# Kernel tuning notes

Measured on AMD Instinct MI355X. Metric: run time of the kernel, lower is better.

The kernel has to match this reference:

```python
import jax, jax.numpy as jnp
import numpy as np

# dims
B, NN, D, HD, L, H, S, FIN = 2048, 64, 128, 128, 4, 8, 8, 16
N = B * NN              # total nodes = 131072
EPG = 8 * NN            # edges per graph (avg degree 8)
E = B * EPG             # total edges = 1048576
A = S * (S - 1)         # num_actions per head = 56


def setup_inputs() -> dict:
    key = jax.random.key(0)
    ks = jax.random.split(key, 16)
    def nrm(k, shape, scale=0.05):
        return jax.random.normal(k, shape, jnp.float32) * scale
    x = jax.random.normal(ks[0], (N, FIN), jnp.float32)
    # per-graph random edges (src/dst local in [0, NN), offset by graph id)
    off = jnp.repeat(jnp.arange(B, dtype=jnp.int32) * NN, EPG)
    src = jax.random.randint(ks[1], (E,), 0, NN, jnp.int32) + off
    dst = jax.random.randint(ks[2], (E,), 0, NN, jnp.int32) + off
    edge_index = jnp.stack([src, dst])
    batch = (jnp.arange(N, dtype=jnp.int32) // NN)
    subsets = jnp.arange(H * S, dtype=jnp.int32).reshape(H, S)
    return dict(
        x=x, edge_index=edge_index, batch=batch, subsets=subsets,
        W_in=nrm(ks[3], (FIN, D)), b_in=jnp.zeros(D, jnp.float32),
        W_self=nrm(ks[4], (L, D, D)), W_nbr=nrm(ks[5], (L, D, D)),
        b_enc=jnp.zeros((L, D), jnp.float32),
        ext_W=nrm(ks[6], (H, 2 * D, HD)), ext_b=jnp.zeros((H, HD), jnp.float32),
        ln_g=jnp.ones((H, HD), jnp.float32), ln_b=jnp.zeros((H, HD), jnp.float32),
        hub_W=nrm(ks[7], (HD, HD)), hub_b=jnp.zeros(HD, jnp.float32),
        pol_W1=nrm(ks[8], (H, 2 * HD, HD)), pol_b1=jnp.zeros((H, HD), jnp.float32),
        pol_W2=nrm(ks[9], (H, HD, A)), pol_b2=jnp.zeros((H, A), jnp.float32),
        val_W1=nrm(ks[10], (D, D)), val_b1=jnp.zeros(D, jnp.float32),
        val_W2=nrm(ks[11], (D, 1)), val_b2=jnp.zeros(1, jnp.float32),
    )


def _forward(floats, edge_index, batch, subsets):
    (x, W_in, b_in, W_self, W_nbr, b_enc, ext_W, ext_b, ln_g, ln_b,
     hub_W, hub_b, pol_W1, pol_b1, pol_W2, pol_b2,
     val_W1, val_b1, val_W2, val_b2) = floats
    src, dst = edge_index[0], edge_index[1]
    # --- GraphEncoder: input proj + L layers of mean-aggregate message passing ---
    deg = jnp.maximum(
        jax.ops.segment_sum(jnp.ones(src.shape[0], x.dtype), dst, num_segments=N), 1.0
    )[:, None]
    h = jax.nn.relu(x @ W_in + b_in)                      # [N, D]
    for l in range(L):
        agg = jax.ops.segment_sum(h[src], dst, num_segments=N) / deg
        h = jax.nn.relu(h @ W_self[l] + agg @ W_nbr[l] + b_enc[l])
    # --- batched per-graph / per-head subset pooling (replaces python loop) ---
    he = h.reshape(B, NN, D)                              # graphs are contiguous in `batch`
    sub = he[:, subsets]                                  # [B, H, S, D]
    pooled = jnp.concatenate([sub.mean(2), sub.max(2)], axis=-1)   # [B, H, 2D]
    z = jnp.einsum('bhf,hfd->bhd', pooled, ext_W) + ext_b
    mu = z.mean(-1, keepdims=True)
    var = z.var(-1, keepdims=True)
    head_emb = jax.nn.relu((z - mu) / jnp.sqrt(var + 1e-5) * ln_g + ln_b)  # [B, H, HD]
    # --- CommunicationHub: shared global context from mean over heads ---
    ctx = jax.nn.relu(head_emb.mean(1) @ hub_W + hub_b)   # [B, HD]
    # --- PolicyHeads: per-head MLP on concat(head_emb, context) ---
    pc = jnp.concatenate(
        [head_emb, jnp.broadcast_to(ctx[:, None, :], head_emb.shape)], axis=-1)
    hh = jax.nn.relu(jnp.einsum('bhf,hfd->bhd', pc, pol_W1) + pol_b1)
    logits = jnp.einsum('bhd,hda->bha', hh, pol_W2) + pol_b2       # [B, H, A]
    # --- ValueHead: per-graph mean pool -> MLP -> tanh ---
    gm = he.mean(1)                                        # segment mean (equal-size graphs)
    v = jnp.tanh(jax.nn.relu(gm @ val_W1 + val_b1) @ val_W2 + val_b2)  # [B, 1]
    return logits, v


def reference(x, edge_index, batch, subsets, W_in, b_in, W_self, W_nbr, b_enc,
              ext_W, ext_b, ln_g, ln_b, hub_W, hub_b, pol_W1, pol_b1, pol_W2,
              pol_b2, val_W1, val_b1, val_W2, val_b2):
    floats = (x, W_in, b_in, W_self, W_nbr, b_enc, ext_W, ext_b, ln_g, ln_b,
              hub_W, hub_b, pol_W1, pol_b1, pol_W2, pol_b2,
              val_W1, val_b1, val_W2, val_b2)
    return _forward(floats, edge_index, batch, subsets)
```

## Files before the change

### kernel.cpp

```cpp
#include <hip/hip_runtime.h>

#define E_TOT 1048576
#define LOGITS 917504

typedef short bf16x8 __attribute__((ext_vector_type(8)));
typedef float f32x4 __attribute__((ext_vector_type(4)));
typedef unsigned short u16;
typedef unsigned int u32;

#define DEV static __device__ __forceinline__

DEV u16 f2bf(float f){ u32 u = __float_as_uint(f); return (u16)((u + 0x7fffu + ((u>>16)&1u))>>16); }
DEV float bf2f(u16 h){ return __uint_as_float(((u32)h)<<16); }
DEV u32 pack2(float a, float b){ return (u32)f2bf(a) | ((u32)f2bf(b)<<16); }
DEV void unpack8(uint4 u, float* f){
  f[0]=__uint_as_float(u.x<<16); f[1]=__uint_as_float(u.x&0xffff0000u);
  f[2]=__uint_as_float(u.y<<16); f[3]=__uint_as_float(u.y&0xffff0000u);
  f[4]=__uint_as_float(u.z<<16); f[5]=__uint_as_float(u.z&0xffff0000u);
  f[6]=__uint_as_float(u.w<<16); f[7]=__uint_as_float(u.w&0xffff0000u);
}
DEV uint4 pack8(const float* f){
  uint4 u; u.x=pack2(f[0],f[1]); u.y=pack2(f[2],f[3]); u.z=pack2(f[4],f[5]); u.w=pack2(f[6],f[7]); return u;
}

#define GNN_E   0
#define EXT_E   131072
#define POL1_E  393216
#define POL2_E  655360
#define HUB_E   720896
#define VW1T_E  737280
#define POOL_E  753664
#define CTX_E   4947968

__global__ __launch_bounds__(256) void pack_w(
    const float* __restrict__ Wself, const float* __restrict__ Wnbr,
    const float* __restrict__ extW,  const float* __restrict__ polW1,
    const float* __restrict__ polW2, const float* __restrict__ hubW,
    const float* __restrict__ valW1, const float* __restrict__ W_in,
    u16* __restrict__ ws)
{
  int idx = blockIdx.x*256 + threadIdx.x;
  if (idx < 131072){
    int l = idx>>15, r = idx&32767;
    int m = (r>>14)&1, r2 = r&16383;
    int kb=(r2>>12)&3, ct=(r2>>9)&7, lane=(r2>>3)&63, j=r2&7;
    int k = kb*32 + ((lane>>4)<<3) + j, n = (ct<<4)+(lane&15);
    const float* W = m? Wnbr : Wself;
    ws[GNN_E+idx] = f2bf(W[(l<<14)+(k<<7)+n]);
  } else if (idx < 655360){
    int i = idx - 131072;
    int isPol = (i >= 262144); if (isPol) i -= 262144;
    int h = i>>15, r = i&32767;
    int kb=(r>>12)&7, ct=(r>>9)&7, lane=(r>>3)&63, j=r&7;
    int k = kb*32 + ((lane>>4)<<3) + j, n = (ct<<4)+(lane&15);
    const float* W = isPol? polW1 : extW;
    ws[(isPol?POL1_E:EXT_E)+i] = f2bf(W[(h<<15)+(k<<7)+n]);
  } else if (idx < 720896){
    int i = idx - 655360;
    int h = i>>13, r = i&8191;
    int kb=(r>>11)&3, ct=(r>>9)&3, lane=(r>>3)&63, j=r&7;
    int k = kb*32+((lane>>4)<<3)+j, n=(ct<<4)+(lane&15);
    float v = (n<56)? polW2[h*7168 + k*56 + n] : 0.0f;
    ws[POL2_E+i] = f2bf(v);
  } else if (idx < 737280){
    int i = idx-720896;
    int kb=(i>>12)&3, ct=(i>>9)&7, lane=(i>>3)&63, j=i&7;
    int k = kb*32+((lane>>4)<<3)+j, n=(ct<<4)+(lane&15);
    ws[HUB_E+i] = f2bf(hubW[(k<<7)+n]);
  } else if (idx < 753664){
    int i = idx-737280;
    int c = i>>7, k = i&127;
    ws[VW1T_E+i] = f2bf(valW1[(k<<7)+c]);
  } else if (idx < 757760){
    int i = idx-753664;
    int ct=(i>>9)&7, lane=(i>>3)&63, j=i&7;
    int k=((lane>>4)<<3)+j, n=(ct<<4)+(lane&15);
    float v = (k<16)? W_in[(k<<7)+n] : 0.0f;
    ws[CTX_E+i] = f2bf(v);
  }
}

DEV void epi_write(u16* h_bf, u16* ht, f32x4 (&acc)[4][2], float b0, float b1,
                   int wv, int r15, int kh)
{
  float bias[2] = {b0, b1};
  #pragma unroll
  for (int rt=0;rt<4;rt++){
    int sch = (rt<<1)+(kh>>1);
    int r0  = (rt<<4)+(kh<<2);
    #pragma unroll
    for (int cc=0;cc<2;cc++){
      int col=(wv<<5)+(cc<<4)+r15;
      float v0=fmaxf(acc[rt][cc][0]+bias[cc],0.0f);
      float v1=fmaxf(acc[rt][cc][1]+bias[cc],0.0f);
      float v2=fmaxf(acc[rt][cc][2]+bias[cc],0.0f);
      float v3=fmaxf(acc[rt][cc][3]+bias[cc],0.0f);
      int chc=(col>>3);
      h_bf[((r0+0)<<7)+(((chc^((r0+0)&7))<<3)|(col&7))]=f2bf(v0);
      h_bf[((r0+1)<<7)+(((chc^((r0+1)&7))<<3)|(col&7))]=f2bf(v1);
      h_bf[((r0+2)<<7)+(((chc^((r0+2)&7))<<3)|(col&7))]=f2bf(v2);
      h_bf[((r0+3)<<7)+(((chc^((r0+3)&7))<<3)|(col&7))]=f2bf(v3);
      uint2 w; w.x=pack2(v0,v1); w.y=pack2(v2,v3);
      *(uint2*)&ht[(col<<6)+(((sch^(col&7))<<3)|((kh&1)<<2))]=w;
    }
  }
}

__global__ __launch_bounds__(256,3) void gnn_kernel(
  const float* __restrict__ x, const int* __restrict__ ei,
  const int* __restrict__ subsets, const float* __restrict__ b_in,
  const float* __restrict__ b_enc, const float* __restrict__ val_b1,
  const float* __restrict__ val_W2, const float* __restrict__ val_b2,
  const u16* __restrict__ packGNN, const u16* __restrict__ packWIN,
  const u16* __restrict__ valW1T,
  u16* __restrict__ pooled, float* __restrict__ out)
{
  __shared__ __align__(16) u16 h_bf[8192];
  __shared__ __align__(16) u16 ht[8192];
  __shared__ __align__(16) u16 agg_bf[8192];
  __shared__ float deg_inv[64];
  __shared__ int subs_s[64];
  __shared__ float redbuf[4];

  int t=threadIdx.x, b=blockIdx.x;
  int lane=t&63, wv=t>>6, r15=lane&15, kh=lane>>4, ctb=wv<<1;
  u32* cnt=(u32*)ht;
  f32x4 zero4={0.0f,0.0f,0.0f,0.0f};

  int e0=(b<<9)+(t<<1);
  int2 sp=*(const int2*)&ei[e0];
  int2 dp=*(const int2*)&ei[E_TOT+e0];
  int s0=sp.x&63, s1=sp.y&63, d0=dp.x&63, d1=dp.y&63;
  if (t<64) subs_s[t]=subsets[t];
  for (int i=t;i<1024;i+=256) ((uint4*)cnt)[i]=make_uint4(0,0,0,0);
  __syncthreads();
  atomicAdd(&cnt[(d0<<6)+((((s0>>3)^(d0&7))<<3)|(s0&7))],1u);
  atomicAdd(&cnt[(d1<<6)+((((s1>>3)^(d1&7))<<3)|(s1&7))],1u);
  __syncthreads();
  if (t<64){
    u32 s=0;
    for (int k2=0;k2<16;k2++){ uint4 v=((uint4*)cnt)[(t<<4)+k2]; s+=v.x+v.y+v.z+v.w; }
    deg_inv[t]=1.0f/(float)(s>0u?s:1u);
  }
  __syncthreads();

  bf16x8 adjf[4][2];
  #pragma unroll
  for (int ct=0;ct<4;ct++){
    int dst=(ct<<4)+r15; float di=deg_inv[dst];
    #pragma unroll
    for (int kb=0;kb<2;kb++){
      int cb=(kb<<2)+kh;
      const u32* p=&cnt[(dst<<6)+((cb^(dst&7))<<3)];
      uint4 lo=*(const uint4*)p, hi=*(const uint4*)(p+4);
      bf16x8 v;
      v[0]=(short)f2bf((float)lo.x*di); v[1]=(short)f2bf((float)lo.y*di);
      v[2]=(short)f2bf((float)lo.z*di); v[3]=(short)f2bf((float)lo.w*di);
      v[4]=(short)f2bf((float)hi.x*di); v[5]=(short)f2bf((float)hi.y*di);
      v[6]=(short)f2bf((float)hi.z*di); v[7]=(short)f2bf((float)hi.w*di);
      adjf[ct][kb]=v;
    }
  }
  u16* xb=agg_bf;
  { const float* xg=x+(b<<10);
    for (int i=t;i<2048;i+=256){
      int row=i>>5, col=i&31;
      float v=(col<16)? xg[(row<<4)+col] : 0.0f;
      xb[(row<<5)+((((col>>3)^(row&3))<<3)|(col&7))]=f2bf(v);
    }
  }
  __syncthreads();

  {
    bf16x8 bw0=*(const bf16x8*)&packWIN[(ctb<<9)+(lane<<3)];
    bf16x8 bw1=*(const bf16x8*)&packWIN[((ctb+1)<<9)+(lane<<3)];
    f32x4 acc[4][2];
    #pragma unroll
    for (int rt=0;rt<4;rt++){ acc[rt][0]=zero4; acc[rt][1]=zero4; }
    #pragma unroll
    for (int rt=0;rt<4;rt++){
      int row=(rt<<4)+r15;
      bf16x8 af=*(const bf16x8*)&xb[(row<<5)+((kh^(row&3))<<3)];
      acc[rt][0]=__builtin_amdgcn_mfma_f32_16x16x32_bf16(af,bw0,acc[rt][0],0,0,0);
      acc[rt][1]=__builtin_amdgcn_mfma_f32_16x16x32_bf16(af,bw1,acc[rt][1],0,0,0);
    }
    float bi0=b_in[(wv<<5)+r15], bi1=b_in[(wv<<5)+16+r15];
    epi_write(h_bf,ht,acc,bi0,bi1,wv,r15,kh);
  }
  __syncthreads();

  #pragma unroll 1
  for (int l=0;l<4;l++){
    const u16* pl = packGNN + (l<<15);
    bf16x8 bs[4][2], bn[4][2];
    #pragma unroll
    for (int kb=0;kb<4;kb++){
      #pragma unroll
      for (int cc=0;cc<2;cc++){
        bs[kb][cc] = *(const bf16x8*)&pl[(kb<<12)+((ctb+cc)<<9)+(lane<<3)];
        bn[kb][cc] = *(const bf16x8*)&pl[16384+(kb<<12)+((ctb+cc)<<9)+(lane<<3)];
      }
    }
    f32x4 a2[2][4];
    #pragma unroll
    for (int rt=0;rt<2;rt++){ a2[rt][0]=zero4; a2[rt][1]=zero4; a2[rt][2]=zero4; a2[rt][3]=zero4; }
    #pragma unroll
    for (int kb=0;kb<2;kb++){
      #pragma unroll
      for (int rt=0;rt<2;rt++){
        int dim=((ctb+rt)<<4)+r15;
        bf16x8 af=*(const bf16x8*)&ht[(dim<<6)+((((kb<<2)+kh)^(dim&7))<<3)];
        #pragma unroll
        for (int ct=0;ct<4;ct++)
          a2[rt][ct]=__builtin_amdgcn_mfma_f32_16x16x32_bf16(af,adjf[ct][kb],a2[rt][ct],0,0,0);
      }
    }
    #pragma unroll
    for (int rt=0;rt<2;rt++){
      int dch=((ctb+rt)<<1)+(kh>>1);
      #pragma unroll
      for (int ct=0;ct<4;ct++){
        int node=(ct<<4)+r15;
        uint2 w; w.x=pack2(a2[rt][ct][0],a2[rt][ct][1]); w.y=pack2(a2[rt][ct][2],a2[rt][ct][3]);
        *(uint2*)&agg_bf[(node<<7)+(((dch^(node&7))<<3)|((kh&1)<<2))]=w;
      }
    }
    __syncthreads();
    f32x4 acc[4][2];
    #pragma unroll
    for (int rt=0;rt<4;rt++){ acc[rt][0]=zero4; acc[rt][1]=zero4; }
    #pragma unroll
    for (int kb=0;kb<4;kb++){
      int ch=(kb<<2)+kh;
      #pragma unroll
      for (int rt=0;rt<4;rt++){
        int row=(rt<<4)+r15;
        bf16x8 af=*(const bf16x8*)&h_bf[(row<<7)+((ch^(row&7))<<3)];
        acc[rt][0]=__builtin_amdgcn_mfma_f32_16x16x32_bf16(af,bs[kb][0],acc[rt][0],0,0,0);
        acc[rt][1]=__builtin_amdgcn_mfma_f32_16x16x32_bf16(af,bs[kb][1],acc[rt][1],0,0,0);
      }
      #pragma unroll
      for (int rt=0;rt<4;rt++){
        int row=(rt<<4)+r15;
        bf16x8 ag=*(const bf16x8*)&agg_bf[(row<<7)+((ch^(row&7))<<3)];
        acc[rt][0]=__builtin_amdgcn_mfma_f32_16x16x32_bf16(ag,bn[kb][0],acc[rt][0],0,0,0);
        acc[rt][1]=__builtin_amdgcn_mfma_f32_16x16x32_bf16(ag,bn[kb][1],acc[rt][1],0,0,0);
      }
    }
    float be0=b_enc[(l<<7)+(wv<<5)+r15], be1=b_enc[(l<<7)+(wv<<5)+16+r15];
    __syncthreads();
    epi_write(h_bf,ht,acc,be0,be1,wv,r15,kh);
    __syncthreads();
  }

  {
    int hd=t>>5, q=t&31, cb=q<<2;
    float ms[4]={0,0,0,0}, mx[4]={-3e38f,-3e38f,-3e38f,-3e38f};
    int ch=cb>>3;
    #pragma unroll
    for (int s=0;s<8;s++){
      int row=subs_s[(hd<<3)+s]; int sw=row&7;
      uint2 u=*(const uint2*)&h_bf[(row<<7)+(((ch^sw)<<3)|(cb&7))];
      float f0=__uint_as_float(u.x<<16), f1=__uint_as_float(u.x&0xffff0000u);
      float f2=__uint_as_float(u.y<<16), f3=__uint_as_float(u.y&0xffff0000u);
      ms[0]+=f0; ms[1]+=f1; ms[2]+=f2; ms[3]+=f3;
      mx[0]=fmaxf(mx[0],f0); mx[1]=fmaxf(mx[1],f1);
      mx[2]=fmaxf(mx[2],f2); mx[3]=fmaxf(mx[3],f3);
    }
    int base=(((b<<3)+hd)<<8);
    uint2 um,ux;
    um.x=pack2(ms[0]*0.125f,ms[1]*0.125f); um.y=pack2(ms[2]*0.125f,ms[3]*0.125f);
    ux.x=pack2(mx[0],mx[1]);               ux.y=pack2(mx[2],mx[3]);
    *(uint2*)&pooled[base+cb]    =um;
    *(uint2*)&pooled[base+128+cb]=ux;
  }
  __syncthreads();

  float* stagef=(float*)agg_bf;
  if (t<128){
    float s=0;
    for (int row=0;row<64;row++)
      s += bf2f(h_bf[(row<<7)+((((t>>3)^(row&7))<<3)|(t&7))]);
    stagef[t]=s*0.015625f;
  }
  __syncthreads();
  if (t<128){
    float acc=val_b1[t];
    const u16* wr=&valW1T[t<<7];
    #pragma unroll 8
    for (int k=0;k<128;k++) acc=fmaf(stagef[k],bf2f(wr[k]),acc);
    float contrib=fmaxf(acc,0.0f)*val_W2[t];
    #pragma unroll
    for (int d=1;d<64;d<<=1) contrib+=__shfl_xor(contrib,d);
    if (lane==0) redbuf[wv]=contrib;
  }
  __syncthreads();
  if (t==0) out[LOGITS+b]=tanhf(redbuf[0]+redbuf[1]+val_b2[0]);
}

__global__ __launch_bounds__(256) void head1_kernel(
  u16* __restrict__ pooled, const u16* __restrict__ packExt,
  const float* __restrict__ ext_b, const float* __restrict__ ln_g,
  const float* __restrict__ ln_b)
{
  __shared__ __align__(16) u16 A_lds[4096];
  __shared__ float zf[16*132];
  int t=threadIdx.x, gb=blockIdx.x, hd=blockIdx.y;
  int lane=t&63, wv=t>>6, r15=lane&15, kh=lane>>4, ctb=wv<<1;
  for (int i=t;i<512;i+=256){
    int row=i>>5, ch=i&31;
    uint4 u=*(const uint4*)&pooled[(((((gb<<4)+row)<<3)+hd)<<8)+(ch<<3)];
    *(uint4*)&A_lds[(row<<8)+((ch^(row&7))<<3)]=u;
  }
  __syncthreads();
  const u16* pw=packExt+(hd<<15);
  bf16x8 bw[8][2];
  #pragma unroll
  for (int kb=0;kb<8;kb++){
    bw[kb][0]=*(const bf16x8*)&pw[(kb<<12)+(ctb<<9)+(lane<<3)];
    bw[kb][1]=*(const bf16x8*)&pw[(kb<<12)+((ctb+1)<<9)+(lane<<3)];
  }
  f32x4 zero4={0.0f,0.0f,0.0f,0.0f};
  f32x4 acc[2]={zero4,zero4};
  #pragma unroll
  for (int kb=0;kb<8;kb++){
    int ch=(kb<<2)+kh;
    bf16x8 a=*(const bf16x8*)&A_lds[(r15<<8)+((ch^(r15&7))<<3)];
    acc[0]=__builtin_amdgcn_mfma_f32_16x16x32_bf16(a,bw[kb][0],acc[0],0,0,0);
    acc[1]=__builtin_amdgcn_mfma_f32_16x16x32_bf16(a,bw[kb][1],acc[1],0,0,0);
  }
  float eb[2]={ext_b[(hd<<7)+(wv<<5)+r15], ext_b[(hd<<7)+(wv<<5)+16+r15]};
  #pragma unroll
  for (int cc=0;cc<2;cc++){
    int col=(wv<<5)+(cc<<4)+r15;
    #pragma unroll
    for (int i=0;i<4;i++) zf[((kh<<2)+i)*132+col]=acc[cc][i]+eb[cc];
  }
  __syncthreads();
  int row=t>>4, q=t&15;
  const float* zr=&zf[row*132+(q<<3)];
  float s=0,ss=0;
  #pragma unroll
  for (int i=0;i<8;i++){ float v=zr[i]; s+=v; ss+=v*v; }
  s+=__shfl_xor(s,1); ss+=__shfl_xor(ss,1);
  s+=__shfl_xor(s,2); ss+=__shfl_xor(ss,2);
  s+=__shfl_xor(s,4); ss+=__shfl_xor(ss,4);
  s+=__shfl_xor(s,8); ss+=__shfl_xor(ss,8);
  float mu=s*0.0078125f, var=ss*0.0078125f-mu*mu, rstd=rsqrtf(var+1e-5f);
  const float* g=&ln_g[(hd<<7)+(q<<3)];
  const float* bb=&ln_b[(hd<<7)+(q<<3)];
  float e[8];
  #pragma unroll
  for (int i=0;i<8;i++) e[i]=fmaxf((zr[i]-mu)*rstd*g[i]+bb[i],0.0f);
  *(uint4*)&pooled[(((((gb<<4)+row)<<3)+hd)<<8)+(q<<3)]=pack8(e);
}

__global__ __launch_bounds__(256) void ctx_kernel(
  const u16* __restrict__ pooled, const u16* __restrict__ packHub,
  const float* __restrict__ hub_b, u16* __restrict__ ctx)
{
  __shared__ __align__(16) u16 m_lds[2048];
  int t=threadIdx.x, gb=blockIdx.x;
  int lane=t&63, wv=t>>6, r15=lane&15, kh=lane>>4, ctb=wv<<1;
  {
    int row=t>>4, ch=t&15;
    float a8[8]={0,0,0,0,0,0,0,0};
    #pragma unroll
    for (int h=0;h<8;h++){
      uint4 u=*(const uint4*)&pooled[(((((gb<<4)+row)<<3)+h)<<8)+(ch<<3)];
      float f[8]; unpack8(u,f);
      #pragma unroll
      for (int k=0;k<8;k++) a8[k]+=f[k];
    }
    #pragma unroll
    for (int k=0;k<8;k++) a8[k]*=0.125f;
    *(uint4*)&m_lds[(row<<7)+((ch^(row&7))<<3)]=pack8(a8);
  }
  __syncthreads();
  bf16x8 bh[4][2];
  #pragma unroll
  for (int kb=0;kb<4;kb++){
    bh[kb][0]=*(const bf16x8*)&packHub[(kb<<12)+(ctb<<9)+(lane<<3)];
    bh[kb][1]=*(const bf16x8*)&packHub[(kb<<12)+((ctb+1)<<9)+(lane<<3)];
  }
  f32x4 zero4={0.0f,0.0f,0.0f,0.0f};
  f32x4 acc[2]={zero4,zero4};
  #pragma unroll
  for (int kb=0;kb<4;kb++){
    int ch=(kb<<2)+kh;
    bf16x8 a=*(const bf16x8*)&m_lds[(r15<<7)+((ch^(r15&7))<<3)];
    acc[0]=__builtin_amdgcn_mfma_f32_16x16x32_bf16(a,bh[kb][0],acc[0],0,0,0);
    acc[1]=__builtin_amdgcn_mfma_f32_16x16x32_bf16(a,bh[kb][1],acc[1],0,0,0);
  }
  float hb[2]={hub_b[(wv<<5)+r15], hub_b[(wv<<5)+16+r15]};
  #pragma unroll
  for (int cc=0;cc<2;cc++){
    int col=(wv<<5)+(cc<<4)+r15;
    #pragma unroll
    for (int i=0;i<4;i++){
      int row=(kh<<2)+i;
      ctx[(((gb<<4)+row)<<7)+col]=f2bf(fmaxf(acc[cc][i]+hb[cc],0.0f));
    }
  }
}

__global__ __launch_bounds__(256) void pol_kernel(
  const u16* __restrict__ pooled, const u16* __restrict__ ctx,
  const u16* __restrict__ packPol1, const u16* __restrict__ packPol2,
  const float* __restrict__ pol_b1, const float* __restrict__ pol_b2,
  float* __restrict__ out)
{
  __shared__ __align__(16) u16 A_lds[4096];
  __shared__ __align__(16) u16 hh[2048];
  int t=threadIdx.x, gb=blockIdx.x, hd=blockIdx.y;
  int lane=t&63, wv=t>>6, r15=lane&15, kh=lane>>4, ctb=wv<<1;
  for (int i=t;i<512;i+=256){
    int row=i>>5, ch=i&31;
    uint4 u;
    if (ch<16) u=*(const uint4*)&pooled[(((((gb<<4)+row)<<3)+hd)<<8)+(ch<<3)];
    else       u=*(const uint4*)&ctx[(((gb<<4)+row)<<7)+((ch-16)<<3)];
    *(uint4*)&A_lds[(row<<8)+((ch^(row&7))<<3)]=u;
  }
  __syncthreads();
  const u16* pw=packPol1+(hd<<15);
  bf16x8 bw[8][2];
  #pragma unroll
  for (int kb=0;kb<8;kb++){
    bw[kb][0]=*(const bf16x8*)&pw[(kb<<12)+(ctb<<9)+(lane<<3)];
    bw[kb][1]=*(const bf16x8*)&pw[(kb<<12)+((ctb+1)<<9)+(lane<<3)];
  }
  f32x4 zero4={0.0f,0.0f,0.0f,0.0f};
  f32x4 acc[2]={zero4,zero4};
  #pragma unroll
  for (int kb=0;kb<8;kb++){
    int ch=(kb<<2)+kh;
    bf16x8 a=*(const bf16x8*)&A_lds[(r15<<8)+((ch^(r15&7))<<3)];
    acc[0]=__builtin_amdgcn_mfma_f32_16x16x32_bf16(a,bw[kb][0],acc[0],0,0,0);
    acc[1]=__builtin_amdgcn_mfma_f32_16x16x32_bf16(a,bw[kb][1],acc[1],0,0,0);
  }
  float pb[2]={pol_b1[(hd<<7)+(wv<<5)+r15], pol_b1[(hd<<7)+(wv<<5)+16+r15]};
  #pragma unroll
  for (int cc=0;cc<2;cc++){
    int col=(wv<<5)+(cc<<4)+r15;
    #pragma unroll
    for (int i=0;i<4;i++){
      int row=(kh<<2)+i;
      float v=fmaxf(acc[cc][i]+pb[cc],0.0f);
      hh[(row<<7)+((((col>>3)^(row&7))<<3)|(col&7))]=f2bf(v);
    }
  }
  __syncthreads();
  const u16* p2=packPol2+(hd<<13);
  bf16x8 b2[4];
  #pragma unroll
  for (int kb=0;kb<4;kb++)
    b2[kb]=*(const bf16x8*)&p2[(kb<<11)+(wv<<9)+(lane<<3)];
  f32x4 a2=zero4;
  #pragma unroll
  for (int kb=0;kb<4;kb++){
    int ch=(kb<<2)+kh;
    bf16x8 a=*(const bf16x8*)&hh[(r15<<7)+((ch^(r15&7))<<3)];
    a2=__builtin_amdgcn_mfma_f32_16x16x32_bf16(a,b2[kb],a2,0,0,0);
  }
  int col=(wv<<4)+r15;
  if (col<56){
    float pb2=pol_b2[hd*56+col];
    #pragma unroll
    for (int i=0;i<4;i++){
      int row=(kh<<2)+i;
      out[(((((gb<<4)+row)<<3)+hd)*56)+col]=a2[i]+pb2;
    }
  }
}

extern "C" void kernel_launch(void* const* d_in, const int* in_sizes, int n_in,
                              void* d_out, int out_size, void* d_ws, size_t ws_size,
                              hipStream_t stream)
{
  const float* x     =(const float*)d_in[0];
  const int*   ei    =(const int*)  d_in[1];
  const int*   subs  =(const int*)  d_in[3];
  const float* W_in  =(const float*)d_in[4];
  const float* b_in  =(const float*)d_in[5];
  const float* W_self=(const float*)d_in[6];
  const float* W_nbr =(const float*)d_in[7];
  const float* b_enc =(const float*)d_in[8];
  const float* extW  =(const float*)d_in[9];
  const float* ext_b =(const float*)d_in[10];
  const float* ln_g  =(const float*)d_in[11];
  const float* ln_b  =(const float*)d_in[12];
  const float* hubW  =(const float*)d_in[13];
  const float* hub_b =(const float*)d_in[14];
  const float* polW1 =(const float*)d_in[15];
  const float* pol_b1=(const float*)d_in[16];
  const float* polW2 =(const float*)d_in[17];
  const float* pol_b2=(const float*)d_in[18];
  const float* valW1 =(const float*)d_in[19];
  const float* val_b1=(const float*)d_in[20];
  const float* valW2 =(const float*)d_in[21];
  const float* val_b2=(const float*)d_in[22];
  float* out=(float*)d_out;
  u16* ws=(u16*)d_ws;

  pack_w<<<2960,256,0,stream>>>(W_self,W_nbr,extW,polW1,polW2,hubW,valW1,W_in,ws);
  gnn_kernel<<<2048,256,0,stream>>>(x,ei,subs,b_in,b_enc,val_b1,valW2,val_b2,
      ws+GNN_E, ws+CTX_E, ws+VW1T_E, ws+POOL_E, out);
  head1_kernel<<<dim3(128,8),256,0,stream>>>(ws+POOL_E, ws+EXT_E, ext_b, ln_g, ln_b);
  ctx_kernel<<<128,256,0,stream>>>(ws+POOL_E, ws+HUB_E, hub_b, ws+CTX_E);
  pol_kernel<<<dim3(128,8),256,0,stream>>>(ws+POOL_E, ws+CTX_E, ws+POL1_E, ws+POL2_E,
      pol_b1, pol_b2, out);
}
```

Before: 218.2 us.

## Vectorize weight packing, x staging, mean pool and value head; stream GNN weights per k-block

Weight packing now has each thread produce eight bf16 values with one 16-byte store, so the pack launch uses one eighth as many blocks. The input-feature staging and value-head dot product switch to vectorized 8-element loads. The graph mean pool reads the transposed ht buffer row-wise instead of strided h_bf, and the pooled mean goes into a dedicated gmbuf. The GNN layer loop loads self and neighbor weight fragments inside the k-block loop instead of preloading all of them, which lowers register pressure but adds global load latency inside the MFMA loop.

```diff
diff --git a/kernel.cpp b/kernel.cpp
--- a/kernel.cpp
+++ b/kernel.cpp
@@ -11,8 +11,8 @@
 #define DEV static __device__ __forceinline__
 
 DEV u16 f2bf(float f){ u32 u = __float_as_uint(f); return (u16)((u + 0x7fffu + ((u>>16)&1u))>>16); }
+DEV u32 pack2(float a, float b){ return (u32)f2bf(a) | ((u32)f2bf(b)<<16); }
 DEV float bf2f(u16 h){ return __uint_as_float(((u32)h)<<16); }
-DEV u32 pack2(float a, float b){ return (u32)f2bf(a) | ((u32)f2bf(b)<<16); }
 DEV void unpack8(uint4 u, float* f){
   f[0]=__uint_as_float(u.x<<16); f[1]=__uint_as_float(u.x&0xffff0000u);
   f[2]=__uint_as_float(u.y<<16); f[3]=__uint_as_float(u.y&0xffff0000u);
@@ -39,44 +39,55 @@
     const float* __restrict__ valW1, const float* __restrict__ W_in,
     u16* __restrict__ ws)
 {
-  int idx = blockIdx.x*256 + threadIdx.x;
+  int idx = (blockIdx.x*256 + threadIdx.x)<<3;
+  float v[8];
   if (idx < 131072){
     int l = idx>>15, r = idx&32767;
     int m = (r>>14)&1, r2 = r&16383;
-    int kb=(r2>>12)&3, ct=(r2>>9)&7, lane=(r2>>3)&63, j=r2&7;
-    int k = kb*32 + ((lane>>4)<<3) + j, n = (ct<<4)+(lane&15);
+    int kb=(r2>>12)&3, ct=(r2>>9)&7, lane=(r2>>3)&63;
+    int k0 = kb*32 + ((lane>>4)<<3), n = (ct<<4)+(lane&15);
     const float* W = m? Wnbr : Wself;
-    ws[GNN_E+idx] = f2bf(W[(l<<14)+(k<<7)+n]);
+    #pragma unroll
+    for (int j=0;j<8;j++) v[j]=W[(l<<14)+((k0+j)<<7)+n];
+    *(uint4*)&ws[GNN_E+idx]=pack8(v);
   } else if (idx < 655360){
     int i = idx - 131072;
     int isPol = (i >= 262144); if (isPol) i -= 262144;
     int h = i>>15, r = i&32767;
-    int kb=(r>>12)&7, ct=(r>>9)&7, lane=(r>>3)&63, j=r&7;
-    int k = kb*32 + ((lane>>4)<<3) + j, n = (ct<<4)+(lane&15);
+    int kb=(r>>12)&7, ct=(r>>9)&7, lane=(r>>3)&63;
+    int k0 = kb*32 + ((lane>>4)<<3), n = (ct<<4)+(lane&15);
     const float* W = isPol? polW1 : extW;
-    ws[(isPol?POL1_E:EXT_E)+i] = f2bf(W[(h<<15)+(k<<7)+n]);
+    #pragma unroll
+    for (int j=0;j<8;j++) v[j]=W[(h<<15)+((k0+j)<<7)+n];
+    *(uint4*)&ws[(isPol?POL1_E:EXT_E)+i]=pack8(v);
   } else if (idx < 720896){
     int i = idx - 655360;
     int h = i>>13, r = i&8191;
-    int kb=(r>>11)&3, ct=(r>>9)&3, lane=(r>>3)&63, j=r&7;
-    int k = kb*32+((lane>>4)<<3)+j, n=(ct<<4)+(lane&15);
-    float v = (n<56)? polW2[h*7168 + k*56 + n] : 0.0f;
-    ws[POL2_E+i] = f2bf(v);
+    int kb=(r>>11)&3, ct=(r>>9)&3, lane=(r>>3)&63;
+    int k0=kb*32+((lane>>4)<<3), n=(ct<<4)+(lane&15);
+    #pragma unroll
+    for (int j=0;j<8;j++) v[j]=(n<56)? polW2[h*7168+(k0+j)*56+n] : 0.0f;
+    *(uint4*)&ws[POL2_E+i]=pack8(v);
   } else if (idx < 737280){
     int i = idx-720896;
-    int kb=(i>>12)&3, ct=(i>>9)&7, lane=(i>>3)&63, j=i&7;
-    int k = kb*32+((lane>>4)<<3)+j, n=(ct<<4)+(lane&15);
-    ws[HUB_E+i] = f2bf(hubW[(k<<7)+n]);
+    int kb=(i>>12)&3, ct=(i>>9)&7, lane=(i>>3)&63;
+    int k0=kb*32+((lane>>4)<<3), n=(ct<<4)+(lane&15);
+    #pragma unroll
+    for (int j=0;j<8;j++) v[j]=hubW[((k0+j)<<7)+n];
+    *(uint4*)&ws[HUB_E+i]=pack8(v);
   } else if (idx < 753664){
     int i = idx-737280;
-    int c = i>>7, k = i&127;
-    ws[VW1T_E+i] = f2bf(valW1[(k<<7)+c]);
+    int c = i>>7, k0 = i&127;
+    #pragma unroll
+    for (int j=0;j<8;j++) v[j]=valW1[((k0+j)<<7)+c];
+    *(uint4*)&ws[VW1T_E+i]=pack8(v);
   } else if (idx < 757760){
     int i = idx-753664;
-    int ct=(i>>9)&7, lane=(i>>3)&63, j=i&7;
-    int k=((lane>>4)<<3)+j, n=(ct<<4)+(lane&15);
-    float v = (k<16)? W_in[(k<<7)+n] : 0.0f;
-    ws[CTX_E+i] = f2bf(v);
+    int ct=(i>>9)&7, lane=(i>>3)&63;
+    int k0=((lane>>4)<<3), n=(ct<<4)+(lane&15);
+    #pragma unroll
+    for (int j=0;j<8;j++) v[j]=(k0+j<16)? W_in[((k0+j)<<7)+n] : 0.0f;
+    *(uint4*)&ws[CTX_E+i]=pack8(v);
   }
 }
 
@@ -120,6 +131,7 @@
   __shared__ __align__(16) u16 agg_bf[8192];
   __shared__ float deg_inv[64];
   __shared__ int subs_s[64];
+  __shared__ float gmbuf[128];
   __shared__ float redbuf[4];
 
   int t=threadIdx.x, b=blockIdx.x;
@@ -139,7 +151,7 @@
   __syncthreads();
   if (t<64){
     u32 s=0;
-    for (int k2=0;k2<16;k2++){ uint4 v=((uint4*)cnt)[(t<<4)+k2]; s+=v.x+v.y+v.z+v.w; }
+    for (int k2=0;k2<16;k2++){ uint4 vv=((uint4*)cnt)[(t<<4)+k2]; s+=vv.x+vv.y+vv.z+vv.w; }
     deg_inv[t]=1.0f/(float)(s>0u?s:1u);
   }
   __syncthreads();
@@ -153,21 +165,27 @@
       int cb=(kb<<2)+kh;
       const u32* p=&cnt[(dst<<6)+((cb^(dst&7))<<3)];
       uint4 lo=*(const uint4*)p, hi=*(const uint4*)(p+4);
-      bf16x8 v;
-      v[0]=(short)f2bf((float)lo.x*di); v[1]=(short)f2bf((float)lo.y*di);
-      v[2]=(short)f2bf((float)lo.z*di); v[3]=(short)f2bf((float)lo.w*di);
-      v[4]=(short)f2bf((float)hi.x*di); v[5]=(short)f2bf((float)hi.y*di);
-      v[6]=(short)f2bf((float)hi.z*di); v[7]=(short)f2bf((float)hi.w*di);
-      adjf[ct][kb]=v;
-    }
-  }
+      uint4 pk;
+      pk.x=pack2((float)lo.x*di,(float)lo.y*di);
+      pk.y=pack2((float)lo.z*di,(float)lo.w*di);
+      pk.z=pack2((float)hi.x*di,(float)hi.y*di);
+      pk.w=pack2((float)hi.z*di,(float)hi.w*di);
+      adjf[ct][kb]=*(bf16x8*)&pk;
+    }
+  }
+
   u16* xb=agg_bf;
-  { const float* xg=x+(b<<10);
-    for (int i=t;i<2048;i+=256){
-      int row=i>>5, col=i&31;
-      float v=(col<16)? xg[(row<<4)+col] : 0.0f;
-      xb[(row<<5)+((((col>>3)^(row&3))<<3)|(col&7))]=f2bf(v);
-    }
+  { int row=t>>2, c0=(t&3)<<3;
+    float v[8];
+    if (c0<16){
+      const float* xg=x+(b<<10)+(row<<4)+c0;
+      #pragma unroll
+      for (int j=0;j<8;j++) v[j]=xg[j];
+    } else {
+      #pragma unroll
+      for (int j=0;j<8;j++) v[j]=0.0f;
+    }
+    *(uint4*)&xb[(row<<5)+((((c0>>3)^(row&3))<<3))]=pack8(v);
   }
   __syncthreads();
 
@@ -192,15 +210,6 @@
   #pragma unroll 1
   for (int l=0;l<4;l++){
     const u16* pl = packGNN + (l<<15);
-    bf16x8 bs[4][2], bn[4][2];
-    #pragma unroll
-    for (int kb=0;kb<4;kb++){
-      #pragma unroll
-      for (int cc=0;cc<2;cc++){
-        bs[kb][cc] = *(const bf16x8*)&pl[(kb<<12)+((ctb+cc)<<9)+(lane<<3)];
-        bn[kb][cc] = *(const bf16x8*)&pl[16384+(kb<<12)+((ctb+cc)<<9)+(lane<<3)];
-      }
-    }
     f32x4 a2[2][4];
     #pragma unroll
     for (int rt=0;rt<2;rt++){ a2[rt][0]=zero4; a2[rt][1]=zero4; a2[rt][2]=zero4; a2[rt][3]=zero4; }
@@ -229,22 +238,26 @@
     f32x4 acc[4][2];
     #pragma unroll
     for (int rt=0;rt<4;rt++){ acc[rt][0]=zero4; acc[rt][1]=zero4; }
-    #pragma unroll
+    #pragma unroll 2
     for (int kb=0;kb<4;kb++){
       int ch=(kb<<2)+kh;
+      bf16x8 bs0=*(const bf16x8*)&pl[(kb<<12)+(ctb<<9)+(lane<<3)];
+      bf16x8 bs1=*(const bf16x8*)&pl[(kb<<12)+((ctb+1)<<9)+(lane<<3)];
+      bf16x8 bn0=*(const bf16x8*)&pl[16384+(kb<<12)+(ctb<<9)+(lane<<3)];
+      bf16x8 bn1=*(const bf16x8*)&pl[16384+(kb<<12)+((ctb+1)<<9)+(lane<<3)];
       #pragma unroll
       for (int rt=0;rt<4;rt++){
         int row=(rt<<4)+r15;
         bf16x8 af=*(const bf16x8*)&h_bf[(row<<7)+((ch^(row&7))<<3)];
-        acc[rt][0]=__builtin_amdgcn_mfma_f32_16x16x32_bf16(af,bs[kb][0],acc[rt][0],0,0,0);
-        acc[rt][1]=__builtin_amdgcn_mfma_f32_16x16x32_bf16(af,bs[kb][1],acc[rt][1],0,0,0);
+        acc[rt][0]=__builtin_amdgcn_mfma_f32_16x16x32_bf16(af,bs0,acc[rt][0],0,0,0);
+        acc[rt][1]=__builtin_amdgcn_mfma_f32_16x16x32_bf16(af,bs1,acc[rt][1],0,0,0);
       }
       #pragma unroll
       for (int rt=0;rt<4;rt++){
         int row=(rt<<4)+r15;
         bf16x8 ag=*(const bf16x8*)&agg_bf[(row<<7)+((ch^(row&7))<<3)];
-        acc[rt][0]=__builtin_amdgcn_mfma_f32_16x16x32_bf16(ag,bn[kb][0],acc[rt][0],0,0,0);
-        acc[rt][1]=__builtin_amdgcn_mfma_f32_16x16x32_bf16(ag,bn[kb][1],acc[rt][1],0,0,0);
+        acc[rt][0]=__builtin_amdgcn_mfma_f32_16x16x32_bf16(ag,bn0,acc[rt][0],0,0,0);
+        acc[rt][1]=__builtin_amdgcn_mfma_f32_16x16x32_bf16(ag,bn1,acc[rt][1],0,0,0);
       }
     }
     float be0=b_enc[(l<<7)+(wv<<5)+r15], be1=b_enc[(l<<7)+(wv<<5)+16+r15];
@@ -274,21 +287,29 @@
     *(uint2*)&pooled[base+cb]    =um;
     *(uint2*)&pooled[base+128+cb]=ux;
   }
-  __syncthreads();
-
-  float* stagef=(float*)agg_bf;
+
+  float gsum=0.0f;
   if (t<128){
-    float s=0;
-    for (int row=0;row<64;row++)
-      s += bf2f(h_bf[(row<<7)+((((t>>3)^(row&7))<<3)|(t&7))]);
-    stagef[t]=s*0.015625f;
-  }
+    #pragma unroll
+    for (int c=0;c<8;c++){
+      uint4 u=*(const uint4*)&ht[(t<<6)+(c<<3)];
+      float f[8]; unpack8(u,f);
+      gsum+=f[0]+f[1]+f[2]+f[3]+f[4]+f[5]+f[6]+f[7];
+    }
+  }
+  __syncthreads();
+  if (t<128) gmbuf[t]=gsum*0.015625f;
   __syncthreads();
   if (t<128){
     float acc=val_b1[t];
-    const u16* wr=&valW1T[t<<7];
-    #pragma unroll 8
-    for (int k=0;k<128;k++) acc=fmaf(stagef[k],bf2f(wr[k]),acc);
+    const uint4* wr=(const uint4*)&valW1T[t<<7];
+    #pragma unroll
+    for (int c=0;c<16;c++){
+      uint4 u=wr[c]; float f[8]; unpack8(u,f);
+      const float* gp=&gmbuf[c<<3];
+      #pragma unroll
+      for (int j=0;j<8;j++) acc=fmaf(gp[j],f[j],acc);
+    }
     float contrib=fmaxf(acc,0.0f)*val_W2[t];
     #pragma unroll
     for (int d=1;d<64;d<<=1) contrib+=__shfl_xor(contrib,d);
@@ -502,7 +523,7 @@
   float* out=(float*)d_out;
   u16* ws=(u16*)d_ws;
 
-  pack_w<<<2960,256,0,stream>>>(W_self,W_nbr,extW,polW1,polW2,hubW,valW1,W_in,ws);
+  pack_w<<<370,256,0,stream>>>(W_self,W_nbr,extW,polW1,polW2,hubW,valW1,W_in,ws);
   gnn_kernel<<<2048,256,0,stream>>>(x,ei,subs,b_in,b_enc,val_b1,valW2,val_b2,
       ws+GNN_E, ws+CTX_E, ws+VW1T_E, ws+POOL_E, out);
   head1_kernel<<<dim3(128,8),256,0,stream>>>(ws+POOL_E, ws+EXT_E, ext_b, ln_g, ln_b);
```

After: 192.3 us. 11.8% less time.
